# Kernel tuning notes

Hardware: AMD Instinct MI355X
Metric: run time of the kernel (lower is better)

## Reference

```python
import jax, jax.numpy as jnp
import numpy as np

# pywt db4 analysis filters (dec_lo, dec_hi), length 8
DEC_LO = np.array([-0.010597401784997278, 0.032883011666982945, 0.030841381835986965,
                   -0.18703481171888114, -0.02798376941698385, 0.6308807679295904,
                   0.7148465705525415, 0.23037781330885523], dtype=np.float32)
DEC_HI = np.array([-0.23037781330885523, 0.7148465705525415, -0.6308807679295904,
                   -0.02798376941698385, 0.18703481171888114, 0.030841381835986965,
                   -0.032883011666982945, -0.010597401784997278], dtype=np.float32)


def setup_inputs() -> dict:
    key = jax.random.key(0)
    x = jax.random.normal(key, (32, 3, 512, 512), dtype=jnp.float32)
    dec = jnp.stack([jnp.asarray(DEC_LO), jnp.asarray(DEC_HI)])  # (2, 8)
    return {"x": x, "dec": dec}


def _afb1d_last(x, dec):
    """Analysis filter bank along last axis: circular pad (end), stride-2
    cross-correlation with lo/hi filters. x: (..., L) -> (lo, hi) each (..., L//2)."""
    L = x.shape[-1]
    taps = dec.shape[-1]
    pad = taps - 1
    xp = jnp.concatenate([x, x[..., :pad]], axis=-1)          # circular pad at end
    flat = xp.reshape(-1, 1, xp.shape[-1])                    # (N, 1, L+pad)
    out = jax.lax.conv_general_dilated(
        flat, dec[:, None, :], window_strides=(2,), padding='VALID',
        dimension_numbers=('NCH', 'OIH', 'NCH'))              # (N, 2, L//2)
    out = out.reshape(*x.shape[:-1], 2, L // 2)
    return out[..., 0, :], out[..., 1, :]


def reference(x, dec):
    B, C, H, W = x.shape
    xr = x.reshape(B * C, H, W)
    # row pass (along W)
    lo_w, hi_w = _afb1d_last(xr, dec)                         # (BC, H, W//2)
    # column pass (along H): move H to last axis
    lo_t = jnp.swapaxes(lo_w, -2, -1)                         # (BC, W//2, H)
    hi_t = jnp.swapaxes(hi_w, -2, -1)
    ll, lh = _afb1d_last(lo_t, dec)                           # (BC, W//2, H//2)
    hl, hh = _afb1d_last(hi_t, dec)
    coeffs = jnp.stack([ll, lh, hl, hh], axis=1)              # (BC, 4, W//2, H//2)
    coeffs = jnp.swapaxes(coeffs, -2, -1)                     # (BC, 4, H//2, W//2)
    return coeffs.reshape(B, C * 4, H // 2, W // 2)
```

## Files before the change

kernel.cpp:

```cpp
#include <hip/hip_runtime.h>


#define TI 8
#define PR (2*TI + 6)
#define HH 512
#define WW 512

typedef float float4u __attribute__((ext_vector_type(4), aligned(8)));
typedef float float2u __attribute__((ext_vector_type(2), aligned(8)));

template <bool CWRAP>
__device__ __forceinline__ void dwt_col(const float* __restrict__ xb,
                                        int rowBase, int c0,
                                        const float* flo, const float* fhi,
                                        float* ll, float* lh, float* hl, float* hh) {
#pragma unroll
    for (int r = 0; r < PR; ++r) {
        int gr = rowBase + r;
        if (gr >= HH) gr -= HH;
        const float* xr = xb + gr * WW;
        float wv[8];
        if constexpr (!CWRAP) {
            float4u a = *(const float4u*)(xr + c0);
            float4u b = *(const float4u*)(xr + c0 + 4);
            wv[0] = a.x; wv[1] = a.y; wv[2] = a.z; wv[3] = a.w;
            wv[4] = b.x; wv[5] = b.y; wv[6] = b.z; wv[7] = b.w;
        } else {
#pragma unroll
            for (int k = 0; k < 4; ++k) {
                int c = c0 + 2 * k;
                if (c >= WW) c -= WW;
                float2u v = *(const float2u*)(xr + c);
                wv[2 * k]     = v.x;
                wv[2 * k + 1] = v.y;
            }
        }
        float rlo = 0.f, rhi = 0.f;
#pragma unroll
        for (int q = 0; q < 8; ++q) { rlo += wv[q] * flo[q]; rhi += wv[q] * fhi[q]; }
#pragma unroll
        for (int p = (r & 1); p < 8; p += 2) {
            int d = r - p;
            if (d >= 0 && d < 2 * TI) {
                int i = d >> 1;
                float cl = flo[p], ch = fhi[p];
                ll[i] += rlo * cl; lh[i] += rlo * ch;
                hl[i] += rhi * cl; hh[i] += rhi * ch;
            }
        }
    }
}

__global__ __launch_bounds__(256)
void dwt2d_db4_kernel(const float* __restrict__ x,
                      const float* __restrict__ dec,
                      float* __restrict__ out) {
    const int tid  = threadIdx.x;
    const int lane = tid & 63;
    const int w    = tid >> 6;

    const int n   = blockIdx.x;
    const int itb = n & 7;
    const int m   = n >> 3;
    const int jt  = m & 3;
    const int bc  = m >> 2;

    const int it = itb * 4 + w;
    const int j  = jt * 64 + lane;
    const int rowBase = it * (2 * TI);
    const int c0 = 2 * j;

    float flo[8], fhi[8];
#pragma unroll
    for (int k = 0; k < 8; ++k) { flo[k] = dec[k]; fhi[k] = dec[8 + k]; }

    const float* xb = x + (size_t)bc * HH * WW;

    float ll[TI], lh[TI], hl[TI], hh[TI];
#pragma unroll
    for (int i = 0; i < TI; ++i) { ll[i] = 0.f; lh[i] = 0.f; hl[i] = 0.f; hh[i] = 0.f; }

    if (jt < 3) dwt_col<false>(xb, rowBase, c0, flo, fhi, ll, lh, hl, hh);
    else        dwt_col<true >(xb, rowBase, c0, flo, fhi, ll, lh, hl, hh);

    const size_t base = ((size_t)(bc * 4) * 256 + (size_t)it * TI) * 256 + j;
#pragma unroll
    for (int i = 0; i < TI; ++i) {
        __builtin_nontemporal_store(ll[i], &out[base + (size_t)i * 256]);
        __builtin_nontemporal_store(lh[i], &out[base + 1 * 65536 + (size_t)i * 256]);
        __builtin_nontemporal_store(hl[i], &out[base + 2 * 65536 + (size_t)i * 256]);
        __builtin_nontemporal_store(hh[i], &out[base + 3 * 65536 + (size_t)i * 256]);
    }
}

extern "C" void kernel_launch(void* const* d_in, const int* in_sizes, int n_in,
                              void* d_out, int out_size, void* d_ws, size_t ws_size,
                              hipStream_t stream) {
    const float* x   = (const float*)d_in[0];
    const float* dec = (const float*)d_in[1];
    float* out = (float*)d_out;

    dim3 grid(8 * 4 * 96);
    dim3 block(256);
    dwt2d_db4_kernel<<<grid, block, 0, stream>>>(x, dec, out);
}
```

Before: 196.6 us.

## Stage input patches in LDS via direct global-to-LDS loads, halve row tile

Each wavefront now copies its input patch (14 rows by 136 columns, wrap handled per 16-byte chunk) into its own LDS region with global_load_lds, then computes the row and column filters from LDS using packed float2 lo/hi math. The row tile shrinks from 8 to 4 output rows, so the grid doubles. The aim is to replace the strided unaligned per-thread global loads with coalesced 16-byte transfers and to drop the separate wraparound path. In exchange, halo rows are re-read more often, the 4x16-byte layout relies on column wrap falling on chunk boundaries, and the LDS use may limit occupancy.

```diff
diff --git a/kernel.cpp b/kernel.cpp
--- a/kernel.cpp
+++ b/kernel.cpp
@@ -1,60 +1,23 @@
 #include <hip/hip_runtime.h>
 
 
-#define TI 8
+#define TI 4
 #define PR (2*TI + 6)
+#define PC 136
+#define NGW (PR * 34)
 #define HH 512
 #define WW 512
 
-typedef float float4u __attribute__((ext_vector_type(4), aligned(8)));
-typedef float float2u __attribute__((ext_vector_type(2), aligned(8)));
-
-template <bool CWRAP>
-__device__ __forceinline__ void dwt_col(const float* __restrict__ xb,
-                                        int rowBase, int c0,
-                                        const float* flo, const float* fhi,
-                                        float* ll, float* lh, float* hl, float* hh) {
-#pragma unroll
-    for (int r = 0; r < PR; ++r) {
-        int gr = rowBase + r;
-        if (gr >= HH) gr -= HH;
-        const float* xr = xb + gr * WW;
-        float wv[8];
-        if constexpr (!CWRAP) {
-            float4u a = *(const float4u*)(xr + c0);
-            float4u b = *(const float4u*)(xr + c0 + 4);
-            wv[0] = a.x; wv[1] = a.y; wv[2] = a.z; wv[3] = a.w;
-            wv[4] = b.x; wv[5] = b.y; wv[6] = b.z; wv[7] = b.w;
-        } else {
-#pragma unroll
-            for (int k = 0; k < 4; ++k) {
-                int c = c0 + 2 * k;
-                if (c >= WW) c -= WW;
-                float2u v = *(const float2u*)(xr + c);
-                wv[2 * k]     = v.x;
-                wv[2 * k + 1] = v.y;
-            }
-        }
-        float rlo = 0.f, rhi = 0.f;
-#pragma unroll
-        for (int q = 0; q < 8; ++q) { rlo += wv[q] * flo[q]; rhi += wv[q] * fhi[q]; }
-#pragma unroll
-        for (int p = (r & 1); p < 8; p += 2) {
-            int d = r - p;
-            if (d >= 0 && d < 2 * TI) {
-                int i = d >> 1;
-                float cl = flo[p], ch = fhi[p];
-                ll[i] += rlo * cl; lh[i] += rlo * ch;
-                hl[i] += rhi * cl; hh[i] += rhi * ch;
-            }
-        }
-    }
-}
+typedef float f2 __attribute__((ext_vector_type(2)));
+typedef const __attribute__((address_space(1))) void gas_t;
+typedef __attribute__((address_space(3))) void las_t;
 
 __global__ __launch_bounds__(256)
 void dwt2d_db4_kernel(const float* __restrict__ x,
                       const float* __restrict__ dec,
                       float* __restrict__ out) {
+    __shared__ __align__(16) float patch[4][PR * PC];
+
     const int tid  = threadIdx.x;
     const int lane = tid & 63;
     const int w    = tid >> 6;
@@ -62,34 +25,69 @@
     const int n   = blockIdx.x;
     const int itb = n & 7;
     const int m   = n >> 3;
-    const int jt  = m & 3;
-    const int bc  = m >> 2;
+    const int s   = m & 1;
+    const int jt  = (m >> 1) & 3;
+    const int bc  = m >> 3;
+    const int it  = (itb * 2 + s) * 4 + w;
 
-    const int it = itb * 4 + w;
-    const int j  = jt * 64 + lane;
     const int rowBase = it * (2 * TI);
-    const int c0 = 2 * j;
+    const int colBase = jt * 128;
 
-    float flo[8], fhi[8];
+    f2 fp[8];
 #pragma unroll
-    for (int k = 0; k < 8; ++k) { flo[k] = dec[k]; fhi[k] = dec[8 + k]; }
+    for (int k = 0; k < 8; ++k) fp[k] = f2{ dec[k], dec[8 + k] };
 
-    const float* xb = x + (size_t)bc * HH * WW;
+    const float* xb  = x + (size_t)bc * HH * WW;
+    float*       smw = patch[w];
 
-    float ll[TI], lh[TI], hl[TI], hh[TI];
 #pragma unroll
-    for (int i = 0; i < TI; ++i) { ll[i] = 0.f; lh[i] = 0.f; hl[i] = 0.f; hh[i] = 0.f; }
+    for (int k = 0; k < 8; ++k) {
+        int g = k * 64 + lane;
+        las_t* lp = (las_t*)((char*)smw + k * 1024);
+        if (g < NGW) {
+            int r  = g / 34;
+            int c4 = g - r * 34;
+            int gr = rowBase + r;      if (gr >= HH) gr -= HH;
+            int gc = colBase + 4 * c4; if (gc >= WW) gc -= WW;
+            __builtin_amdgcn_global_load_lds((gas_t*)(xb + gr * WW + gc), lp, 16, 0, 0);
+        }
+    }
+    asm volatile("s_waitcnt vmcnt(0)" ::: "memory");
+    __builtin_amdgcn_sched_barrier(0);
 
-    if (jt < 3) dwt_col<false>(xb, rowBase, c0, flo, fhi, ll, lh, hl, hh);
-    else        dwt_col<true >(xb, rowBase, c0, flo, fhi, ll, lh, hl, hh);
+    f2 aL[TI], aH[TI];
+#pragma unroll
+    for (int i = 0; i < TI; ++i) { aL[i] = f2{0.f, 0.f}; aH[i] = f2{0.f, 0.f}; }
 
-    const size_t base = ((size_t)(bc * 4) * 256 + (size_t)it * TI) * 256 + j;
+#pragma unroll
+    for (int r = 0; r < PR; ++r) {
+        const f2* row = (const f2*)&smw[r * PC];
+        f2 a = row[lane];     f2 b = row[lane + 1];
+        f2 c = row[lane + 2]; f2 d = row[lane + 3];
+        float wv[8] = { a.x, a.y, b.x, b.y, c.x, c.y, d.x, d.y };
+        f2 rf = fp[0] * wv[0];
+#pragma unroll
+        for (int q = 1; q < 8; ++q) rf += fp[q] * wv[q];
+#pragma unroll
+        for (int p = (r & 1); p < 8; p += 2) {
+            int dd = r - p;
+            if (dd >= 0 && dd < 2 * TI) {
+                int i = dd >> 1;
+                aL[i] += fp[p] * rf.x;
+                aH[i] += fp[p] * rf.y;
+            }
+        }
+    }
+
+    const int oi = it * TI;
+    const int oj = jt * 64 + lane;
+    const size_t base = ((size_t)(bc * 4) * 256 + oi) * 256 + oj;
 #pragma unroll
     for (int i = 0; i < TI; ++i) {
-        __builtin_nontemporal_store(ll[i], &out[base + (size_t)i * 256]);
-        __builtin_nontemporal_store(lh[i], &out[base + 1 * 65536 + (size_t)i * 256]);
-        __builtin_nontemporal_store(hl[i], &out[base + 2 * 65536 + (size_t)i * 256]);
-        __builtin_nontemporal_store(hh[i], &out[base + 3 * 65536 + (size_t)i * 256]);
+        __builtin_nontemporal_store(aL[i].x, &out[base + (size_t)i * 256]);
+        __builtin_nontemporal_store(aL[i].y, &out[base + 1 * 65536 + (size_t)i * 256]);
+        __builtin_nontemporal_store(aH[i].x, &out[base + 2 * 65536 + (size_t)i * 256]);
+        __builtin_nontemporal_store(aH[i].y, &out[base + 3 * 65536 + (size_t)i * 256]);
     }
 }
 
@@ -100,7 +98,7 @@
     const float* dec = (const float*)d_in[1];
     float* out = (float*)d_out;
 
-    dim3 grid(8 * 4 * 96);
+    dim3 grid(8 * 2 * 4 * 96);
     dim3 block(256);
     dwt2d_db4_kernel<<<grid, block, 0, stream>>>(x, dec, out);
 }
```

Result: faster. 174.2 us (-11.4%).
